# Performance work log

Hardware: AMD Instinct MI355X
Metric: run time of the kernel (lower is better)

Reference implementation:

```python
import jax, jax.numpy as jnp
import numpy as np

POOL = (7, 7, 3)          # (py, px, pz) pool_size
N_LEVELS = 4              # pyramid_levels = [0,1,2,3]


def setup_inputs() -> dict:
    key = jax.random.key(0)
    ks = jax.random.split(key, 8)
    B, C = 2, 48
    shapes = [(96, 96, 48), (48, 48, 24), (24, 24, 12), (12, 12, 6)]
    fm = {f"fmap{i}": jax.random.normal(ks[i], (B, C) + shapes[i], jnp.float32)
          for i in range(N_LEVELS)}
    N = 1200
    ctr = jax.random.uniform(ks[4], (N, 3), minval=0.15, maxval=0.85)
    sz = jax.random.uniform(ks[5], (N, 3), minval=0.05, maxval=0.5)
    lo = jnp.clip(ctr - sz / 2, 0.0, 1.0)
    hi = jnp.clip(ctr + sz / 2, 0.0, 1.0)
    bix = jax.random.randint(ks[6], (N,), 0, B).astype(jnp.float32)
    # rois: (N, (y1, x1, y2, x2, z1, z2, batch_ix)) normalized coords
    rois = jnp.stack([lo[:, 0], lo[:, 1], hi[:, 0], hi[:, 1],
                      lo[:, 2], hi[:, 2], bix], axis=1)
    return {**fm, "rois": rois}


def _roi_align_3d(fmap, boxes, bix, pool):
    """fmap: (B,C,Y,X,Z); boxes: (N,6) in fmap pixel coords; bix: (N,) int32.
    Trilinear roi_align, sampling one point per bin center. Returns (N,C,py,px,pz)."""
    B, C, Y, X, Z = fmap.shape
    py, px, pz = pool
    N = boxes.shape[0]
    y1, x1, y2, x2, z1, z2 = (boxes[:, i] for i in range(6))

    def centers(a, b, n):
        binsz = (b - a) / n
        return a[:, None] + (jnp.arange(n, dtype=boxes.dtype) + 0.5) * binsz[:, None]

    ys = centers(y1, y2, py)  # (N, py)
    xs = centers(x1, x2, px)  # (N, px)
    zs = centers(z1, z2, pz)  # (N, pz)
    S = py * px * pz
    yy = jnp.broadcast_to(ys[:, :, None, None], (N, py, px, pz)).reshape(N, S)
    xx = jnp.broadcast_to(xs[:, None, :, None], (N, py, px, pz)).reshape(N, S)
    zz = jnp.broadcast_to(zs[:, None, None, :], (N, py, px, pz)).reshape(N, S)

    valid = ((yy > -1.0) & (yy < Y) & (xx > -1.0) & (xx < X)
             & (zz > -1.0) & (zz < Z))
    yc = jnp.clip(yy, 0.0, Y - 1)
    xc = jnp.clip(xx, 0.0, X - 1)
    zc = jnp.clip(zz, 0.0, Z - 1)

    y0 = jnp.floor(yc).astype(jnp.int32); y1i = jnp.minimum(y0 + 1, Y - 1)
    x0 = jnp.floor(xc).astype(jnp.int32); x1i = jnp.minimum(x0 + 1, X - 1)
    z0 = jnp.floor(zc).astype(jnp.int32); z1i = jnp.minimum(z0 + 1, Z - 1)
    ly = yc - y0; hy = 1.0 - ly
    lx = xc - x0; hx = 1.0 - lx
    lz = zc - z0; hz = 1.0 - lz

    fm = jnp.transpose(fmap, (0, 2, 3, 4, 1))  # (B,Y,X,Z,C)
    b = jnp.broadcast_to(bix[:, None], (N, S))

    def g(yi, xi, zi):
        return fm[b, yi, xi, zi]  # (N,S,C)

    val = (g(y0, x0, z0) * (hy * hx * hz)[..., None]
           + g(y0, x0, z1i) * (hy * hx * lz)[..., None]
           + g(y0, x1i, z0) * (hy * lx * hz)[..., None]
           + g(y0, x1i, z1i) * (hy * lx * lz)[..., None]
           + g(y1i, x0, z0) * (ly * hx * hz)[..., None]
           + g(y1i, x0, z1i) * (ly * hx * lz)[..., None]
           + g(y1i, x1i, z0) * (ly * lx * hz)[..., None]
           + g(y1i, x1i, z1i) * (ly * lx * lz)[..., None])
    val = jnp.where(valid[..., None], val, 0.0)
    return jnp.transpose(val.reshape(N, py, px, pz, C), (0, 4, 1, 2, 3))


def reference(fmap0, fmap1, fmap2, fmap3, rois):
    fmaps = [fmap0, fmap1, fmap2, fmap3]
    boxes = rois[:, :6]
    bix = rois[:, 6].astype(jnp.int32)
    h = boxes[:, 2] - boxes[:, 0]
    w = boxes[:, 3] - boxes[:, 1]
    # roi_level = round(4 + log2(sqrt(h*w))).clamp(levels[0], levels[-1])
    roi_level = jnp.clip(jnp.round(4.0 + 0.5 * jnp.log2(h * w)),
                         0, N_LEVELS - 1).astype(jnp.int32)
    out = jnp.zeros((rois.shape[0], fmap0.shape[1]) + POOL, rois.dtype)
    for lvl, fmap in enumerate(fmaps):
        Y, X, Z = fmap.shape[2:]
        scale = jnp.array([Y, X, Y, X, Z, Z], dtype=rois.dtype)
        pooled = _roi_align_3d(fmap, boxes * scale, bix, POOL)
        sel = (roi_level == lvl)[:, None, None, None, None]
        out = out + jnp.where(sel, pooled, 0.0)
    # Equivalent to the torch code's per-level index_select + concat + sort
    # reassembly: output is in original roi order.
    return out
```

## Files before the change

### kernel.cpp

```cpp
#include <hip/hip_runtime.h>

#define PY 7
#define PX 7
#define PZ 3
#define S_BINS 147
#define C_CH   48
#define PER_ROI 7056

__global__ __launch_bounds__(256) void roialign3d_kernel(
    const float* __restrict__ f0, const float* __restrict__ f1,
    const float* __restrict__ f2, const float* __restrict__ f3,
    const float* __restrict__ rois, float* __restrict__ out, int total_bins)
{
    int t = blockIdx.x * blockDim.x + threadIdx.x;
    if (t >= total_bins) return;

    unsigned n = (unsigned)t / S_BINS;
    unsigned s = (unsigned)t - n * S_BINS;

    const float* r = rois + n * 7;
    float by1 = r[0], bx1 = r[1], by2 = r[2], bx2 = r[3], bz1 = r[4], bz2 = r[5];
    int b = (int)r[6];

    float h = by2 - by1, w = bx2 - bx1;
    float lv = rintf(4.0f + 0.5f * log2f(h * w));
    lv = fminf(fmaxf(lv, 0.0f), 3.0f);
    int level = (int)lv;

    const float* fm; int Y, X, Z;
    switch (level) {
        case 0: fm = f0; Y = 96; X = 96; Z = 48; break;
        case 1: fm = f1; Y = 48; X = 48; Z = 24; break;
        case 2: fm = f2; Y = 24; X = 24; Z = 12; break;
        default: fm = f3; Y = 12; X = 12; Z = 6;  break;
    }

    int ybin = s / (PX * PZ);
    int rs   = s - ybin * (PX * PZ);
    int xbin = rs / PZ;
    int zbin = rs - xbin * PZ;

    float fy1 = by1 * Y, fy2 = by2 * Y;
    float fx1 = bx1 * X, fx2 = bx2 * X;
    float fz1 = bz1 * Z, fz2 = bz2 * Z;

    float yy = fy1 + (ybin + 0.5f) * (fy2 - fy1) * (1.0f / PY);
    float xx = fx1 + (xbin + 0.5f) * (fx2 - fx1) * (1.0f / PX);
    float zz = fz1 + (zbin + 0.5f) * (fz2 - fz1) * (1.0f / PZ);

    bool valid = (yy > -1.0f) && (yy < (float)Y) &&
                 (xx > -1.0f) && (xx < (float)X) &&
                 (zz > -1.0f) && (zz < (float)Z);

    float yc = fminf(fmaxf(yy, 0.0f), (float)(Y - 1));
    float xc = fminf(fmaxf(xx, 0.0f), (float)(X - 1));
    float zc = fminf(fmaxf(zz, 0.0f), (float)(Z - 1));

    int y0 = (int)floorf(yc);
    int x0 = (int)floorf(xc);
    int z0 = (int)floorf(zc);
    int y1i = min(y0 + 1, Y - 1);
    int x1i = min(x0 + 1, X - 1);

    float ly = yc - (float)y0, lx = xc - (float)x0, lz = zc - (float)z0;
    float hy = 1.0f - ly,      hx = 1.0f - lx,      hz = 1.0f - lz;

    int  zb    = min(z0, Z - 2);
    bool shift = (zb != z0);
    float wlo  = shift ? 0.0f : hz;
    float whi  = shift ? 1.0f : lz;
    if (!valid) { wlo = 0.0f; whi = 0.0f; }

    float w00 = hy * hx, w01 = hy * lx, w10 = ly * hx, w11 = ly * lx;

    const int plane = Y * X * Z;
    const float* base = fm + (size_t)b * C_CH * plane;

    const float* p00 = base + (y0  * X + x0 ) * Z + zb;
    const float* p01 = base + (y0  * X + x1i) * Z + zb;
    const float* p10 = base + (y1i * X + x0 ) * Z + zb;
    const float* p11 = base + (y1i * X + x1i) * Z + zb;

    float* op = out + (size_t)n * PER_ROI + s;

    #pragma unroll 4
    for (int c = 0; c < C_CH; ++c) {
        float2 v00 = *(const float2*)p00;
        float2 v01 = *(const float2*)p01;
        float2 v10 = *(const float2*)p10;
        float2 v11 = *(const float2*)p11;

        float lo = w00 * v00.x + w01 * v01.x + w10 * v10.x + w11 * v11.x;
        float hi = w00 * v00.y + w01 * v01.y + w10 * v10.y + w11 * v11.y;
        float val = wlo * lo + whi * hi;

        __builtin_nontemporal_store(val, op);

        p00 += plane; p01 += plane; p10 += plane; p11 += plane;
        op += S_BINS;
    }
}

extern "C" void kernel_launch(void* const* d_in, const int* in_sizes, int n_in,
                              void* d_out, int out_size, void* d_ws, size_t ws_size,
                              hipStream_t stream) {
    const float* f0   = (const float*)d_in[0];
    const float* f1   = (const float*)d_in[1];
    const float* f2   = (const float*)d_in[2];
    const float* f3   = (const float*)d_in[3];
    const float* rois = (const float*)d_in[4];
    float* out = (float*)d_out;

    int n_rois = out_size / PER_ROI;
    int total_bins = n_rois * S_BINS;
    int block = 256;
    int grid  = (total_bins + block - 1) / block;
    roialign3d_kernel<<<grid, block, 0, stream>>>(f0, f1, f2, f3, rois, out, total_bins);
}
```

Measured before the change: 35.79 us.

## Share xy-bilinear gathers across z bins and split channels into thread slices

Each thread now handles one (y,x) bin for a 12-channel slice and all three z bins, instead of one (y,x,z) bin for all 48 channels. When the three z-bin corner pairs fall inside one or two aligned 4-wide windows, the four xy corners are fetched as float4 vectors and reduced once. The z interpolation is then applied as small weight vectors, with a fallback path that does per-bin float2 gathers. The goal is fewer redundant gather loads and more parallelism per ROI. The cost is extra branching, more registers, and possibly misaligned float4 loads when zq is not a multiple of 4.

```diff
diff --git a/kernel.cpp b/kernel.cpp
--- a/kernel.cpp
+++ b/kernel.cpp
@@ -6,17 +6,27 @@
 #define S_BINS 147
 #define C_CH   48
 #define PER_ROI 7056
+#define CPT 12
+#define QPR 49
+#define TPR 196
+
+typedef float vf2 __attribute__((ext_vector_type(2)));
+typedef float vf4 __attribute__((ext_vector_type(4)));
 
 __global__ __launch_bounds__(256) void roialign3d_kernel(
-    const float* __restrict__ f0, const float* __restrict__ f1,
-    const float* __restrict__ f2, const float* __restrict__ f3,
-    const float* __restrict__ rois, float* __restrict__ out, int total_bins)
+    const float* __restrict__ fm0, const float* __restrict__ fm1,
+    const float* __restrict__ fm2, const float* __restrict__ fm3,
+    const float* __restrict__ rois, float* __restrict__ out, int total)
 {
     int t = blockIdx.x * blockDim.x + threadIdx.x;
-    if (t >= total_bins) return;
-
-    unsigned n = (unsigned)t / S_BINS;
-    unsigned s = (unsigned)t - n * S_BINS;
+    if (t >= total) return;
+
+    unsigned n  = (unsigned)t / TPR;
+    unsigned r2 = (unsigned)t - n * TPR;
+    unsigned cs = r2 / QPR;
+    unsigned q  = r2 - cs * QPR;
+    unsigned ybin = q / PX;
+    unsigned xbin = q - ybin * PX;
 
     const float* r = rois + n * 7;
     float by1 = r[0], bx1 = r[1], by2 = r[2], bx2 = r[3], bz1 = r[4], bz2 = r[5];
@@ -29,75 +39,165 @@
 
     const float* fm; int Y, X, Z;
     switch (level) {
-        case 0: fm = f0; Y = 96; X = 96; Z = 48; break;
-        case 1: fm = f1; Y = 48; X = 48; Z = 24; break;
-        case 2: fm = f2; Y = 24; X = 24; Z = 12; break;
-        default: fm = f3; Y = 12; X = 12; Z = 6;  break;
-    }
-
-    int ybin = s / (PX * PZ);
-    int rs   = s - ybin * (PX * PZ);
-    int xbin = rs / PZ;
-    int zbin = rs - xbin * PZ;
+        case 0: fm = fm0; Y = 96; X = 96; Z = 48; break;
+        case 1: fm = fm1; Y = 48; X = 48; Z = 24; break;
+        case 2: fm = fm2; Y = 24; X = 24; Z = 12; break;
+        default: fm = fm3; Y = 12; X = 12; Z = 6;  break;
+    }
 
     float fy1 = by1 * Y, fy2 = by2 * Y;
     float fx1 = bx1 * X, fx2 = bx2 * X;
-    float fz1 = bz1 * Z, fz2 = bz2 * Z;
-
     float yy = fy1 + (ybin + 0.5f) * (fy2 - fy1) * (1.0f / PY);
     float xx = fx1 + (xbin + 0.5f) * (fx2 - fx1) * (1.0f / PX);
-    float zz = fz1 + (zbin + 0.5f) * (fz2 - fz1) * (1.0f / PZ);
-
-    bool valid = (yy > -1.0f) && (yy < (float)Y) &&
-                 (xx > -1.0f) && (xx < (float)X) &&
-                 (zz > -1.0f) && (zz < (float)Z);
+
+    bool vy = (yy > -1.0f) && (yy < (float)Y);
+    bool vx = (xx > -1.0f) && (xx < (float)X);
+    float xyv = (vy && vx) ? 1.0f : 0.0f;
 
     float yc = fminf(fmaxf(yy, 0.0f), (float)(Y - 1));
     float xc = fminf(fmaxf(xx, 0.0f), (float)(X - 1));
-    float zc = fminf(fmaxf(zz, 0.0f), (float)(Z - 1));
-
     int y0 = (int)floorf(yc);
     int x0 = (int)floorf(xc);
-    int z0 = (int)floorf(zc);
     int y1i = min(y0 + 1, Y - 1);
     int x1i = min(x0 + 1, X - 1);
-
-    float ly = yc - (float)y0, lx = xc - (float)x0, lz = zc - (float)z0;
-    float hy = 1.0f - ly,      hx = 1.0f - lx,      hz = 1.0f - lz;
-
-    int  zb    = min(z0, Z - 2);
-    bool shift = (zb != z0);
-    float wlo  = shift ? 0.0f : hz;
-    float whi  = shift ? 1.0f : lz;
-    if (!valid) { wlo = 0.0f; whi = 0.0f; }
-
-    float w00 = hy * hx, w01 = hy * lx, w10 = ly * hx, w11 = ly * lx;
+    float ly = yc - (float)y0, lx = xc - (float)x0;
+    float hy = 1.0f - ly,      hx = 1.0f - lx;
+
+    float w00 = hy * hx * xyv, w01 = hy * lx * xyv;
+    float w10 = ly * hx * xyv, w11 = ly * lx * xyv;
+
+    float fz1 = bz1 * Z, fz2 = bz2 * Z;
+    float bsz = (fz2 - fz1) * (1.0f / PZ);
+    int zb0, zb1, zb2;
+    float wlo0, whi0, wlo1, whi1, wlo2, whi2;
+    {
+        float zz, zc, lz; int z0i, zb; bool vz, shift; float wl, wh;
+        #define ZBIN(i, ZB, WL, WH) \
+            zz = fz1 + ((i) + 0.5f) * bsz; \
+            vz = (zz > -1.0f) && (zz < (float)Z); \
+            zc = fminf(fmaxf(zz, 0.0f), (float)(Z - 1)); \
+            z0i = (int)floorf(zc); \
+            lz = zc - (float)z0i; \
+            zb = min(z0i, Z - 2); \
+            shift = (zb != z0i); \
+            wl = (shift ? 0.0f : (1.0f - lz)); \
+            wh = (shift ? 1.0f : lz); \
+            if (!vz) { wl = 0.0f; wh = 0.0f; } \
+            ZB = zb; WL = wl; WH = wh;
+        ZBIN(0, zb0, wlo0, whi0)
+        ZBIN(1, zb1, wlo1, whi1)
+        ZBIN(2, zb2, wlo2, whi2)
+        #undef ZBIN
+    }
 
     const int plane = Y * X * Z;
-    const float* base = fm + (size_t)b * C_CH * plane;
-
-    const float* p00 = base + (y0  * X + x0 ) * Z + zb;
-    const float* p01 = base + (y0  * X + x1i) * Z + zb;
-    const float* p10 = base + (y1i * X + x0 ) * Z + zb;
-    const float* p11 = base + (y1i * X + x1i) * Z + zb;
-
-    float* op = out + (size_t)n * PER_ROI + s;
-
-    #pragma unroll 4
-    for (int c = 0; c < C_CH; ++c) {
-        float2 v00 = *(const float2*)p00;
-        float2 v01 = *(const float2*)p01;
-        float2 v10 = *(const float2*)p10;
-        float2 v11 = *(const float2*)p11;
-
-        float lo = w00 * v00.x + w01 * v01.x + w10 * v10.x + w11 * v11.x;
-        float hi = w00 * v00.y + w01 * v01.y + w10 * v10.y + w11 * v11.y;
-        float val = wlo * lo + whi * hi;
-
-        __builtin_nontemporal_store(val, op);
-
-        p00 += plane; p01 += plane; p10 += plane; p11 += plane;
-        op += S_BINS;
+    const float* base = fm + ((size_t)b * C_CH + cs * CPT) * (size_t)plane;
+    const int o00 = (y0  * X + x0 ) * Z;
+    const int o01 = (y0  * X + x1i) * Z;
+    const int o10 = (y1i * X + x0 ) * Z;
+    const int o11 = (y1i * X + x1i) * Z;
+
+    unsigned s = ybin * (PX * PZ) + xbin * PZ;
+    float* op = out + (size_t)n * PER_ROI + (size_t)cs * CPT * S_BINS + s;
+
+    int zq = min(zb0, Z - 4);
+    int dA2 = zb2 - zq;
+    bool pathA = (dA2 <= 2);
+
+    if (pathA) {
+        int d0 = zb0 - zq, d1 = zb1 - zq, d2 = zb2 - zq;
+        float W0[4], W1[4], W2[4];
+        #pragma unroll
+        for (int j = 0; j < 4; ++j) {
+            W0[j] = (j == d0) ? wlo0 : (j == d0 + 1) ? whi0 : 0.0f;
+            W1[j] = (j == d1) ? wlo1 : (j == d1 + 1) ? whi1 : 0.0f;
+            W2[j] = (j == d2) ? wlo2 : (j == d2 + 1) ? whi2 : 0.0f;
+        }
+        const float* p00 = base + o00 + zq;
+        const float* p01 = base + o01 + zq;
+        const float* p10 = base + o10 + zq;
+        const float* p11 = base + o11 + zq;
+        #pragma unroll 2
+        for (int c = 0; c < CPT; ++c) {
+            vf4 r00 = *(const vf4*)p00;
+            vf4 r01 = *(const vf4*)p01;
+            vf4 r10 = *(const vf4*)p10;
+            vf4 r11 = *(const vf4*)p11;
+            float rs0 = w00*r00[0] + w01*r01[0] + w10*r10[0] + w11*r11[0];
+            float rs1 = w00*r00[1] + w01*r01[1] + w10*r10[1] + w11*r11[1];
+            float rs2 = w00*r00[2] + w01*r01[2] + w10*r10[2] + w11*r11[2];
+            float rs3 = w00*r00[3] + w01*r01[3] + w10*r10[3] + w11*r11[3];
+            __builtin_nontemporal_store(W0[0]*rs0 + W0[1]*rs1 + W0[2]*rs2 + W0[3]*rs3, op + 0);
+            __builtin_nontemporal_store(W1[0]*rs0 + W1[1]*rs1 + W1[2]*rs2 + W1[3]*rs3, op + 1);
+            __builtin_nontemporal_store(W2[0]*rs0 + W2[1]*rs1 + W2[2]*rs2 + W2[3]*rs3, op + 2);
+            p00 += plane; p01 += plane; p10 += plane; p11 += plane;
+            op += S_BINS;
+        }
+        return;
+    }
+
+    int zB = zb2 - 2;
+    bool d1inA = (zb1 - zq) <= 2;
+    bool d1inB = (zb1 >= zB);
+    bool pathB = d1inA || d1inB;
+
+    if (pathB) {
+        int d0 = zb0 - zq;
+        int d1 = d1inA ? (zb1 - zq) : (4 + zb1 - zB);
+        int d2 = 6;
+        float W0[8], W1[8], W2[8];
+        #pragma unroll
+        for (int j = 0; j < 8; ++j) {
+            W0[j] = (j == d0) ? wlo0 : (j == d0 + 1) ? whi0 : 0.0f;
+            W1[j] = (j == d1) ? wlo1 : (j == d1 + 1) ? whi1 : 0.0f;
+            W2[j] = (j == d2) ? wlo2 : (j == d2 + 1) ? whi2 : 0.0f;
+        }
+        const float* p00 = base + o00; const float* p01 = base + o01;
+        const float* p10 = base + o10; const float* p11 = base + o11;
+        for (int c = 0; c < CPT; ++c) {
+            vf4 a00 = *(const vf4*)(p00 + zq), b00v = *(const vf4*)(p00 + zB);
+            vf4 a01 = *(const vf4*)(p01 + zq), b01v = *(const vf4*)(p01 + zB);
+            vf4 a10 = *(const vf4*)(p10 + zq), b10v = *(const vf4*)(p10 + zB);
+            vf4 a11 = *(const vf4*)(p11 + zq), b11v = *(const vf4*)(p11 + zB);
+            float rs[8];
+            #pragma unroll
+            for (int j = 0; j < 4; ++j) {
+                rs[j]     = w00*a00[j] + w01*a01[j] + w10*a10[j] + w11*a11[j];
+                rs[4 + j] = w00*b00v[j] + w01*b01v[j] + w10*b10v[j] + w11*b11v[j];
+            }
+            float v0 = 0.0f, v1 = 0.0f, v2 = 0.0f;
+            #pragma unroll
+            for (int j = 0; j < 8; ++j) {
+                v0 += W0[j] * rs[j]; v1 += W1[j] * rs[j]; v2 += W2[j] * rs[j];
+            }
+            __builtin_nontemporal_store(v0, op + 0);
+            __builtin_nontemporal_store(v1, op + 1);
+            __builtin_nontemporal_store(v2, op + 2);
+            p00 += plane; p01 += plane; p10 += plane; p11 += plane;
+            op += S_BINS;
+        }
+        return;
+    }
+
+    {
+        const float* p00 = base + o00; const float* p01 = base + o01;
+        const float* p10 = base + o10; const float* p11 = base + o11;
+        for (int c = 0; c < CPT; ++c) {
+            #define BIN(ZB, WL, WH, OFS) { \
+                vf2 v00 = *(const vf2*)(p00 + ZB); \
+                vf2 v01 = *(const vf2*)(p01 + ZB); \
+                vf2 v10 = *(const vf2*)(p10 + ZB); \
+                vf2 v11 = *(const vf2*)(p11 + ZB); \
+                float lo = w00*v00[0] + w01*v01[0] + w10*v10[0] + w11*v11[0]; \
+                float hi = w00*v00[1] + w01*v01[1] + w10*v10[1] + w11*v11[1]; \
+                __builtin_nontemporal_store(WL*lo + WH*hi, op + OFS); }
+            BIN(zb0, wlo0, whi0, 0)
+            BIN(zb1, wlo1, whi1, 1)
+            BIN(zb2, wlo2, whi2, 2)
+            #undef BIN
+            p00 += plane; p01 += plane; p10 += plane; p11 += plane;
+            op += S_BINS;
+        }
     }
 }
 
@@ -112,8 +212,8 @@
     float* out = (float*)d_out;
 
     int n_rois = out_size / PER_ROI;
-    int total_bins = n_rois * S_BINS;
-    int block = 256;
-    int grid  = (total_bins + block - 1) / block;
-    roialign3d_kernel<<<grid, block, 0, stream>>>(f0, f1, f2, f3, rois, out, total_bins);
+    int total  = n_rois * TPR;
+    int block  = 256;
+    int grid   = (total + block - 1) / block;
+    roialign3d_kernel<<<grid, block, 0, stream>>>(f0, f1, f2, f3, rois, out, total);
 }
```

Result: slower. 56.77 us (+58.6%).
